# Performance work log

Hardware: AMD Instinct MI355X
Metric: run time of the kernel (lower is better)

Reference implementation:

```python
import jax, jax.numpy as jnp
import numpy as np
from jax import lax


def _lstm_last(x, Wih, Whh, bih, bhh):
    """Single-layer torch-style LSTM (gate order i,f,g,o); returns last hidden state.
    x: (M, T, F) -> (M, H)."""
    gx = jnp.einsum('mtf,gf->mtg', x, Wih) + bih + bhh  # precompute input contributions
    H = Whh.shape[1]
    Wh = Whh.T
    def step(carry, g):
        h, c = carry
        z = g + h @ Wh
        i, f, gg, o = jnp.split(z, 4, axis=-1)
        c = jax.nn.sigmoid(f) * c + jax.nn.sigmoid(i) * jnp.tanh(gg)
        h = jax.nn.sigmoid(o) * jnp.tanh(c)
        return (h, c), None
    M = x.shape[0]
    init = (jnp.zeros((M, H), x.dtype), jnp.zeros((M, H), x.dtype))
    (h, _), _ = lax.scan(step, init, jnp.swapaxes(gx, 0, 1))
    return h


def _forward(input_data, rel_encoding, lstm_Wih, lstm_Whh, lstm_bih, lstm_bhh,
             hop_w1, hop_b1, hop_w2, hop_b2, fn_w1, fn_b1, fn_w2, fn_b2):
    B, W, N, F = input_data.shape
    U = lstm_Whh.shape[1]
    # SequentialEmbedding: per-stock LSTM over the window, take last step
    x = jnp.transpose(input_data, (0, 2, 1, 3)).reshape(B * N, W, F)
    seq = _lstm_last(x, lstm_Wih, lstm_Whh, lstm_bih, lstm_bhh).reshape(B, N, U)

    # RelationalEmbedding: dense N x N k-hop message passing
    mask = (rel_encoding.sum(-1) > 0).astype(seq.dtype)  # (N,N)
    D = mask.sum(-1)                                      # (N,) degrees (self-loops keep >0)
    e = seq
    for k in range(hop_w1.shape[0]):  # k_hops: small fixed loop
        W1 = hop_w1[k]
        # mask * concat([e_i, e_j, enc]) @ W1 + b1, computed blockwise without
        # materializing the (B,N,N,2U+K) concat; mask scales only the pre-bias term
        xi = e @ W1[:U]                                    # (B,N,INP)
        xj = e @ W1[U:2 * U]                               # (B,N,INP)
        xe = jnp.einsum('ijk,kp->ijp', rel_encoding, W1[2 * U:])  # (N,N,INP)
        pre = mask[None, :, :, None] * (xi[:, :, None, :] + xj[:, None, :, :] + xe[None]) + hop_b1[k]
        hdn = jax.nn.leaky_relu(pre)                       # (B,N,N,INP)
        wts = jax.nn.leaky_relu(hdn @ hop_w2[k] + hop_b2[k])[..., 0]  # (B,N,N)
        scaled = (wts * mask) / D[None, :, None]
        # torch: sum_i scaled[b,i,j] * e_j  ==  e_j * (sum_i scaled[b,i,j])
        e = scaled.sum(axis=1)[..., None] * e

    # FullyConnected head: Linear(2U,2U)+LeakyReLU, Linear(2U,1)+LeakyReLU, squeeze
    comb = jnp.concatenate([seq, e], axis=-1)              # (B,N,2U)
    out = jax.nn.leaky_relu(comb @ fn_w1 + fn_b1)
    out = jax.nn.leaky_relu(out @ fn_w2 + fn_b2)
    return out[..., 0]                                     # (B,N)


def setup_inputs() -> dict:
    key = jax.random.key(0)
    ks = jax.random.split(key, 14)
    B, W, N, F = 2, 32, 768, 4
    U, K, KH = 32, 8, 2
    INP = 2 * U + K  # 72
    def w(k, shape, fan):
        return jax.random.normal(k, shape, jnp.float32) / np.float32(np.sqrt(fan))
    enc = (jax.random.uniform(ks[1], (N, N, K)) < 0.05).astype(jnp.float32)
    # self-loops in relation channel 0 so every node has degree >= 1
    enc = enc.at[:, :, 0].set(jnp.maximum(enc[:, :, 0], jnp.eye(N, dtype=jnp.float32)))
    return {
        'input_data': jax.random.normal(ks[0], (B, W, N, F), jnp.float32),
        'rel_encoding': enc,
        'lstm_Wih': w(ks[2], (4 * U, F), F),
        'lstm_Whh': w(ks[3], (4 * U, U), U),
        'lstm_bih': 0.01 * jax.random.normal(ks[4], (4 * U,), jnp.float32),
        'lstm_bhh': 0.01 * jax.random.normal(ks[5], (4 * U,), jnp.float32),
        'hop_w1': w(ks[6], (KH, INP, INP), INP),
        'hop_b1': 0.01 * jax.random.normal(ks[7], (KH, INP), jnp.float32),
        'hop_w2': w(ks[8], (KH, INP, 1), INP),
        'hop_b2': 0.01 * jax.random.normal(ks[9], (KH, 1), jnp.float32),
        'fn_w1': w(ks[10], (2 * U, 2 * U), 2 * U),
        'fn_b1': 0.01 * jax.random.normal(ks[11], (2 * U,), jnp.float32),
        'fn_w2': w(ks[12], (2 * U, 1), 2 * U),
        'fn_b2': 0.01 * jax.random.normal(ks[13], (1,), jnp.float32),
    }


def reference(input_data, rel_encoding, lstm_Wih, lstm_Whh, lstm_bih, lstm_bhh,
              hop_w1, hop_b1, hop_w2, hop_b2, fn_w1, fn_b1, fn_w2, fn_b2):
    return _forward(input_data, rel_encoding, lstm_Wih, lstm_Whh, lstm_bih, lstm_bhh,
                    hop_w1, hop_b1, hop_w2, hop_b2, fn_w1, fn_b1, fn_w2, fn_b2)
```

## Files before the change

kernel.cpp:

```cpp
#include <hip/hip_runtime.h>

#define N_STK 768
#define BATCH 2
#define WIN   32
#define FEAT  4
#define UNITS 32
#define INP   72
#define LROW  76
#define NSLC  19
#define IPH   64
#define JCR   24
#define NPHI  12
#define NCR   32

__device__ __forceinline__ float lrelu(float v){ return v > 0.0f ? v : 0.01f*v; }
__device__ __forceinline__ float lanebcast(float v, int l){
    return __int_as_float(__builtin_amdgcn_readlane(__float_as_int(v), l));
}
__device__ __forceinline__ unsigned patof(const float* __restrict__ p){
    float4 a = *reinterpret_cast<const float4*>(p);
    float4 b = *reinterpret_cast<const float4*>(p + 4);
    unsigned m = 0;
    m |= (a.x != 0.0f) ? 1u   : 0u;
    m |= (a.y != 0.0f) ? 2u   : 0u;
    m |= (a.z != 0.0f) ? 4u   : 0u;
    m |= (a.w != 0.0f) ? 8u   : 0u;
    m |= (b.x != 0.0f) ? 16u  : 0u;
    m |= (b.y != 0.0f) ? 32u  : 0u;
    m |= (b.z != 0.0f) ? 64u  : 0u;
    m |= (b.w != 0.0f) ? 128u : 0u;
    return m;
}
__device__ __forceinline__ void async_cp16(const float* g, float* l){
    __builtin_amdgcn_global_load_lds(
        (const __attribute__((address_space(1))) unsigned int*)g,
        (__attribute__((address_space(3))) unsigned int*)l,
        16, 0, 0);
}

__global__ __launch_bounds__(256) void k1_kernel(const float* __restrict__ rel,
        const float* __restrict__ x, const float* __restrict__ Wih,
        const float* __restrict__ Whh, const float* __restrict__ bih,
        const float* __restrict__ bhh, const float* __restrict__ hop_w1,
        const float* __restrict__ hop_b1,
        float* __restrict__ seq, float* __restrict__ invD,
        unsigned char* __restrict__ Pout,
        float* __restrict__ lutlo, float* __restrict__ luthi,
        float* __restrict__ xi0, float* __restrict__ xj0,
        float* __restrict__ s0){
    int j = blockIdx.x, tid = threadIdx.x;
    int wv = tid >> 6, lane = tid & 63;
    __shared__ float hrow[2][UNITS];
    __shared__ int cw_sh[2];

    if (wv < 2){
        int b = wv;
        int r0 = lane, r1 = 64 + lane;
        bool low = (lane < 32);
        float4 wi0 = *reinterpret_cast<const float4*>(Wih + r0*FEAT);
        float4 wi1 = *reinterpret_cast<const float4*>(Wih + r1*FEAT);
        float bb0 = bih[r0] + bhh[r0];
        float bb1 = bih[r1] + bhh[r1];
        float4 W0[8], W1[8];
        #pragma unroll
        for (int q = 0; q < 8; q++){
            W0[q] = *reinterpret_cast<const float4*>(Whh + r0*UNITS + q*4);
            W1[q] = *reinterpret_cast<const float4*>(Whh + r1*UNITS + q*4);
        }
        float4 xv = make_float4(0.f, 0.f, 0.f, 0.f);
        if (low) xv = *reinterpret_cast<const float4*>(x + ((size_t)(b*WIN + lane)*N_STK + j)*FEAT);
        float hreg = 0.0f, c = 0.0f;
        #pragma unroll 1
        for (int t = 0; t < WIN; t++){
            float xb0 = lanebcast(xv.x, t), xb1 = lanebcast(xv.y, t);
            float xb2 = lanebcast(xv.z, t), xb3 = lanebcast(xv.w, t);
            float z0a = bb0 + wi0.x*xb0 + wi0.z*xb2;
            float z0b =       wi0.y*xb1 + wi0.w*xb3;
            float z1a = bb1 + wi1.x*xb0 + wi1.z*xb2;
            float z1b =       wi1.y*xb1 + wi1.w*xb3;
            #pragma unroll
            for (int q = 0; q < 8; q++){
                float h0 = lanebcast(hreg, 32 + q*4 + 0);
                float h1 = lanebcast(hreg, 32 + q*4 + 1);
                float h2 = lanebcast(hreg, 32 + q*4 + 2);
                float h3 = lanebcast(hreg, 32 + q*4 + 3);
                z0a += W0[q].x*h0; z0b += W0[q].y*h1;
                z0a += W0[q].z*h2; z0b += W0[q].w*h3;
                z1a += W1[q].x*h0; z1b += W1[q].y*h1;
                z1a += W1[q].z*h2; z1b += W1[q].w*h3;
            }
            float z0 = z0a + z0b, z1 = z1a + z1b;
            float e0 = __expf(-z0);
            float s0g = 1.0f/(1.0f + e0);
            float sc = low ? -2.0f : -1.0f;
            float e1 = __expf(sc*z1);
            float rr = 1.0f/(1.0f + e1);
            float act = low ? (1.0f - e1)*rr : rr;
            float pa = s0g*act;
            float po = __shfl_xor(pa, 32);
            c = s0g*c + po;
            float e2 = __expf(-2.0f*c);
            float th = (1.0f - e2)/(1.0f + e2);
            hreg = act*th;
        }
        if (!low){
            hrow[b][lane - 32] = hreg;
            seq[((size_t)b*N_STK + j)*UNITS + (lane - 32)] = hreg;
        }
    } else {
        int half = wv - 2;
        int local = 0;
        #pragma unroll
        for (int k = 0; k < 6; k++){
            int col = half*384 + k*64 + lane;
            unsigned p = patof(rel + ((size_t)j*N_STK + col)*8);
            Pout[(size_t)j*N_STK + col] = (unsigned char)p;
            local += p ? 1 : 0;
        }
        #pragma unroll
        for (int d = 32; d; d >>= 1) local += __shfl_xor(local, d);
        if (lane == 0) cw_sh[half] = local;
    }
    __syncthreads();
    if (tid == 0){
        invD[j] = 1.0f/(float)(cw_sh[0] + cw_sh[1]);
        s0[j] = 0.0f; s0[N_STK + j] = 0.0f;
    }
    if (j < 64 && tid >= 144 && tid < 216){
        int p = tid - 144;
        int m = j & 15, half = (j >> 4) & 1, k = j >> 5;
        const float* W = hop_w1 + (size_t)k*INP*INP;
        float acc = half ? 0.0f : hop_b1[k*INP + p];
        int base = 2*UNITS + (half ? 4 : 0);
        #pragma unroll
        for (int q = 0; q < 4; q++)
            if ((m >> q) & 1) acc += W[(base + q)*INP + p];
        (half ? luthi : lutlo)[(k*16 + m)*INP + p] = acc;
    }
    if (tid < 2*INP){
        int b = tid/INP, p = tid - b*INP;
        float si = 0.0f, sj = 0.0f;
        #pragma unroll
        for (int u = 0; u < UNITS; u++){
            float ev = hrow[b][u];
            si += ev * hop_w1[u*INP + p];
            sj += ev * hop_w1[(UNITS + u)*INP + p];
        }
        size_t o = ((size_t)b*N_STK + j)*INP + p;
        xi0[o] = si; xj0[o] = sj;
    }
}

__global__ __launch_bounds__(256) void hop_kernel(const float* __restrict__ xi,
        const float* __restrict__ xj,
        const float* __restrict__ lutlo_k, const float* __restrict__ luthi_k,
        const float* __restrict__ w2, const float* __restrict__ b2,
        const unsigned char* __restrict__ P, const float* __restrict__ invD,
        float* __restrict__ s_out){
    int cr = blockIdx.x, ip = blockIdx.y, b = blockIdx.z;
    int j0 = cr*JCR, i0 = ip*IPH, tid = threadIdx.x;
    __shared__ float xi_sh[IPH*LROW];
    __shared__ float xj_sh[JCR*LROW];
    __shared__ float lo_sh[16*LROW];
    __shared__ float hi_sh[16*LROW];
    __shared__ float invD_sh[IPH];
    __shared__ float acc_sh[JCR];
    __shared__ unsigned elist[IPH*JCR];
    __shared__ int lcnt;

    const float* xib = xi + ((size_t)b*N_STK + i0)*INP;
    const float* xjb = xj + ((size_t)b*N_STK + j0)*INP;

    if (tid == 0) lcnt = 0;
    if (tid < JCR) acc_sh[tid] = 0.0f;
    __syncthreads();

    for (int u = tid; u < IPH*NSLC; u += 256){
        int r = u/NSLC, sl = u - r*NSLC;
        int off = (sl < 18) ? sl*4 : 0;
        async_cp16(xib + (size_t)r*INP + off, &xi_sh[0] + (size_t)u*4);
    }
    for (int u = tid; u < JCR*NSLC; u += 256){
        int r = u/NSLC, sl = u - r*NSLC;
        int off = (sl < 18) ? sl*4 : 0;
        async_cp16(xjb + (size_t)r*INP + off, &xj_sh[0] + (size_t)u*4);
    }
    for (int u = tid; u < 16*NSLC; u += 256){
        int r = u/NSLC, sl = u - r*NSLC;
        int off = (sl < 18) ? sl*4 : 0;
        async_cp16(lutlo_k + r*INP + off, &lo_sh[0] + (size_t)u*4);
    }
    for (int u = tid; u < 16*NSLC; u += 256){
        int r = u/NSLC, sl = u - r*NSLC;
        int off = (sl < 18) ? sl*4 : 0;
        async_cp16(luthi_k + r*INP + off, &hi_sh[0] + (size_t)u*4);
    }
    if (tid < IPH/4) async_cp16(invD + i0 + tid*4, &invD_sh[0] + tid*4);

    if (tid < IPH){
        const unsigned* prow = reinterpret_cast<const unsigned*>(P + (size_t)(i0 + tid)*N_STK + j0);
        unsigned w[6];
        #pragma unroll
        for (int k = 0; k < 6; k++) w[k] = prow[k];
        #pragma unroll
        for (int k = 0; k < 24; k++){
            unsigned pat = (w[k >> 2] >> ((k & 3)*8)) & 255u;
            if (pat){
                int pos = atomicAdd(&lcnt, 1);
                elist[pos] = ((unsigned)tid << 13) | ((unsigned)k << 8) | pat;
            }
        }
    }

    int hf = tid & 1;
    float4 w2r[9];
    #pragma unroll
    for (int q = 0; q < 9; q++) w2r[q] = *reinterpret_cast<const float4*>(w2 + hf*36 + q*4);
    float b2v = b2[0];
    __syncthreads();

    int m = lcnt;
    for (int sl = tid >> 1; sl < m; sl += 128){
        unsigned ent = elist[sl];
        int il = ent >> 13, jl = (ent >> 8) & 31;
        int mlo = (int)(ent & 15u), mhi = (int)((ent >> 4) & 15u);
        const float* xr = &xi_sh[il*LROW + hf*36];
        const float* jr = &xj_sh[jl*LROW + hf*36];
        const float* lr = &lo_sh[mlo*LROW + hf*36];
        const float* hr = &hi_sh[mhi*LROW + hf*36];
        float dot = 0.0f;
        #pragma unroll
        for (int q = 0; q < 9; q++){
            float4 xv = *reinterpret_cast<const float4*>(xr + q*4);
            float4 jv = *reinterpret_cast<const float4*>(jr + q*4);
            float4 lv = *reinterpret_cast<const float4*>(lr + q*4);
            float4 hv = *reinterpret_cast<const float4*>(hr + q*4);
            float4 w  = w2r[q];
            dot += lrelu(xv.x + jv.x + lv.x + hv.x)*w.x;
            dot += lrelu(xv.y + jv.y + lv.y + hv.y)*w.y;
            dot += lrelu(xv.z + jv.z + lv.z + hv.z)*w.z;
            dot += lrelu(xv.w + jv.w + lv.w + hv.w)*w.w;
        }
        dot += __shfl_xor(dot, 1);
        if (hf == 0) atomicAdd(&acc_sh[jl], lrelu(dot + b2v)*invD_sh[il]);
    }
    __syncthreads();
    if (tid < JCR) atomicAdd(&s_out[b*N_STK + j0 + tid], acc_sh[tid]);
}

template<int MODE>
__global__ __launch_bounds__(192) void ep_kernel(const float* __restrict__ sview,
        const float* __restrict__ ein, const float* __restrict__ seqg,
        float* __restrict__ eout,
        const float* __restrict__ W1next, float* __restrict__ xi_next,
        float* __restrict__ xj_next, float* __restrict__ s_next,
        const float* __restrict__ fw1, const float* __restrict__ fb1,
        const float* __restrict__ fw2, const float* __restrict__ fb2,
        float* __restrict__ outp){
    int j = blockIdx.x, tid = threadIdx.x;
    __shared__ float e_sh[2][64];
    if (tid < 64){
        int b = tid >> 5, u = tid & 31;
        size_t o = ((size_t)b*N_STK + j)*UNITS + u;
        float ev = ein[o]*sview[b*N_STK + j];
        if (MODE == 0){ e_sh[b][u] = ev; eout[o] = ev; }
        else          { e_sh[b][32 + u] = ev; e_sh[b][u] = seqg[o]; }
    }
    if (MODE == 0 && tid >= 160 && tid < 162) s_next[(tid - 160)*N_STK + j] = 0.0f;
    __syncthreads();
    if (MODE == 0){
        if (tid < 2*INP){
            int b = tid/INP, p = tid - b*INP;
            float si = 0.0f, sj = 0.0f;
            #pragma unroll
            for (int u = 0; u < UNITS; u++){
                float ev = e_sh[b][u];
                si += ev * W1next[u*INP + p];
                sj += ev * W1next[(UNITS + u)*INP + p];
            }
            size_t o = ((size_t)b*N_STK + j)*INP + p;
            xi_next[o] = si; xj_next[o] = sj;
        }
    } else {
        if (tid < 128){
            int b = tid >> 6, u = tid & 63;
            float acc = fb1[u];
            #pragma unroll 8
            for (int d = 0; d < 64; d++) acc += e_sh[b][d]*fw1[d*64 + u];
            float prod = lrelu(acc)*fw2[u];
            prod += __shfl_xor(prod, 32);
            prod += __shfl_xor(prod, 16);
            prod += __shfl_xor(prod, 8);
            prod += __shfl_xor(prod, 4);
            prod += __shfl_xor(prod, 2);
            prod += __shfl_xor(prod, 1);
            if (u == 0) outp[b*N_STK + j] = lrelu(prod + fb2[0]);
        }
    }
}

extern "C" void kernel_launch(void* const* d_in, const int* in_sizes, int n_in,
                              void* d_out, int out_size, void* d_ws, size_t ws_size,
                              hipStream_t stream){
    const float* input_data = (const float*)d_in[0];
    const float* rel        = (const float*)d_in[1];
    const float* lstm_Wih   = (const float*)d_in[2];
    const float* lstm_Whh   = (const float*)d_in[3];
    const float* lstm_bih   = (const float*)d_in[4];
    const float* lstm_bhh   = (const float*)d_in[5];
    const float* hop_w1     = (const float*)d_in[6];
    const float* hop_b1     = (const float*)d_in[7];
    const float* hop_w2     = (const float*)d_in[8];
    const float* hop_b2     = (const float*)d_in[9];
    const float* fn_w1      = (const float*)d_in[10];
    const float* fn_b1      = (const float*)d_in[11];
    const float* fn_w2      = (const float*)d_in[12];
    const float* fn_b2      = (const float*)d_in[13];
    float* out = (float*)d_out;

    float* ws    = (float*)d_ws;
    float* seq   = ws;
    float* eA    = seq   + 49152;
    float* xi0   = eA    + 49152;
    float* xj0   = xi0   + 110592;
    float* xi1   = xj0   + 110592;
    float* xj1   = xi1   + 110592;
    float* lutlo = xj1   + 110592;
    float* luthi = lutlo + 2304;
    float* invD  = luthi + 2304;
    float* s0    = invD  + 768;
    float* s1    = s0    + 1536;
    unsigned char* P = (unsigned char*)(s1 + 1536);

    k1_kernel<<<N_STK, 256, 0, stream>>>(rel, input_data, lstm_Wih, lstm_Whh,
            lstm_bih, lstm_bhh, hop_w1, hop_b1,
            seq, invD, P, lutlo, luthi, xi0, xj0, s0);

    dim3 hgrid(NCR, NPHI, BATCH);
    hop_kernel<<<hgrid, 256, 0, stream>>>(xi0, xj0, lutlo, luthi,
            hop_w2, hop_b2, P, invD, s0);

    ep_kernel<0><<<N_STK, 192, 0, stream>>>(s0, seq, nullptr, eA,
            hop_w1 + INP*INP, xi1, xj1, s1,
            nullptr, nullptr, nullptr, nullptr, nullptr);

    hop_kernel<<<hgrid, 256, 0, stream>>>(xi1, xj1, lutlo + 16*INP, luthi + 16*INP,
            hop_w2 + INP, hop_b2 + 1, P, invD, s1);

    ep_kernel<1><<<N_STK, 192, 0, stream>>>(s1, eA, seq, nullptr,
            nullptr, nullptr, nullptr, nullptr,
            fn_w1, fn_b1, fn_w2, fn_b2, out);
}
```

Measured before the change: 148.6 us.

## Fuse epilogue kernels into hop kernel via last-block counter and split edge lists

Removes the two separate epilogue kernel launches by having the last hop block for each column range (found with a global atomic counter after a threadfence) run the epilogue work for its 24 columns. The edge list is now built with a deterministic wave prefix scan, split into low-only patterns (one LUT row) and patterns that need both LUTs, so low-only edges skip the second LUT lookup. Counter and s1 zeroing move into k1. This trades launch overhead for serialized tail work in a few blocks and adds atomic and fence costs.

```diff
diff --git a/kernel.cpp b/kernel.cpp
--- a/kernel.cpp
+++ b/kernel.cpp
@@ -47,7 +47,8 @@
         unsigned char* __restrict__ Pout,
         float* __restrict__ lutlo, float* __restrict__ luthi,
         float* __restrict__ xi0, float* __restrict__ xj0,
-        float* __restrict__ s0){
+        float* __restrict__ s0, float* __restrict__ s1,
+        int* __restrict__ cnt0, int* __restrict__ cnt1){
     int j = blockIdx.x, tid = threadIdx.x;
     int wv = tid >> 6, lane = tid & 63;
     __shared__ float hrow[2][UNITS];
@@ -91,14 +92,14 @@
             }
             float z0 = z0a + z0b, z1 = z1a + z1b;
             float e0 = __expf(-z0);
-            float s0g = 1.0f/(1.0f + e0);
+            float sg = 1.0f/(1.0f + e0);
             float sc = low ? -2.0f : -1.0f;
             float e1 = __expf(sc*z1);
             float rr = 1.0f/(1.0f + e1);
             float act = low ? (1.0f - e1)*rr : rr;
-            float pa = s0g*act;
+            float pa = sg*act;
             float po = __shfl_xor(pa, 32);
-            c = s0g*c + po;
+            c = sg*c + po;
             float e2 = __expf(-2.0f*c);
             float th = (1.0f - e2)/(1.0f + e2);
             hreg = act*th;
@@ -113,9 +114,9 @@
         #pragma unroll
         for (int k = 0; k < 6; k++){
             int col = half*384 + k*64 + lane;
-            unsigned p = patof(rel + ((size_t)j*N_STK + col)*8);
-            Pout[(size_t)j*N_STK + col] = (unsigned char)p;
-            local += p ? 1 : 0;
+            unsigned pt = patof(rel + ((size_t)j*N_STK + col)*8);
+            Pout[(size_t)j*N_STK + col] = (unsigned char)pt;
+            local += pt ? 1 : 0;
         }
         #pragma unroll
         for (int d = 32; d; d >>= 1) local += __shfl_xor(local, d);
@@ -125,38 +126,47 @@
     if (tid == 0){
         invD[j] = 1.0f/(float)(cw_sh[0] + cw_sh[1]);
         s0[j] = 0.0f; s0[N_STK + j] = 0.0f;
-    }
+        s1[j] = 0.0f; s1[N_STK + j] = 0.0f;
+    }
+    if (j < 64 && tid == 1){ cnt0[j] = 0; cnt1[j] = 0; }
     if (j < 64 && tid >= 144 && tid < 216){
-        int p = tid - 144;
+        int pp = tid - 144;
         int m = j & 15, half = (j >> 4) & 1, k = j >> 5;
         const float* W = hop_w1 + (size_t)k*INP*INP;
-        float acc = half ? 0.0f : hop_b1[k*INP + p];
+        float acc = half ? 0.0f : hop_b1[k*INP + pp];
         int base = 2*UNITS + (half ? 4 : 0);
         #pragma unroll
         for (int q = 0; q < 4; q++)
-            if ((m >> q) & 1) acc += W[(base + q)*INP + p];
-        (half ? luthi : lutlo)[(k*16 + m)*INP + p] = acc;
+            if ((m >> q) & 1) acc += W[(base + q)*INP + pp];
+        (half ? luthi : lutlo)[(k*16 + m)*INP + pp] = acc;
     }
     if (tid < 2*INP){
-        int b = tid/INP, p = tid - b*INP;
+        int b = tid/INP, pp = tid - b*INP;
         float si = 0.0f, sj = 0.0f;
         #pragma unroll
         for (int u = 0; u < UNITS; u++){
             float ev = hrow[b][u];
-            si += ev * hop_w1[u*INP + p];
-            sj += ev * hop_w1[(UNITS + u)*INP + p];
-        }
-        size_t o = ((size_t)b*N_STK + j)*INP + p;
+            si += ev * hop_w1[u*INP + pp];
+            sj += ev * hop_w1[(UNITS + u)*INP + pp];
+        }
+        size_t o = ((size_t)b*N_STK + j)*INP + pp;
         xi0[o] = si; xj0[o] = sj;
     }
 }
 
+template<int MODE>
 __global__ __launch_bounds__(256) void hop_kernel(const float* __restrict__ xi,
         const float* __restrict__ xj,
         const float* __restrict__ lutlo_k, const float* __restrict__ luthi_k,
         const float* __restrict__ w2, const float* __restrict__ b2,
         const unsigned char* __restrict__ P, const float* __restrict__ invD,
-        float* __restrict__ s_out){
+        float* __restrict__ s_out, int* __restrict__ cnt,
+        const float* __restrict__ seqg, float* __restrict__ eA,
+        const float* __restrict__ W1next, float* __restrict__ xi_next,
+        float* __restrict__ xj_next,
+        const float* __restrict__ fw1, const float* __restrict__ fb1,
+        const float* __restrict__ fw2, const float* __restrict__ fb2,
+        float* __restrict__ outp){
     int cr = blockIdx.x, ip = blockIdx.y, b = blockIdx.z;
     int j0 = cr*JCR, i0 = ip*IPH, tid = threadIdx.x;
     __shared__ float xi_sh[IPH*LROW];
@@ -165,15 +175,13 @@
     __shared__ float hi_sh[16*LROW];
     __shared__ float invD_sh[IPH];
     __shared__ float acc_sh[JCR];
+    __shared__ float sarr[JCR];
     __shared__ unsigned elist[IPH*JCR];
-    __shared__ int lcnt;
+    __shared__ int n0_sh, nt_sh, isLast;
 
     const float* xib = xi + ((size_t)b*N_STK + i0)*INP;
     const float* xjb = xj + ((size_t)b*N_STK + j0)*INP;
-
-    if (tid == 0) lcnt = 0;
-    if (tid < JCR) acc_sh[tid] = 0.0f;
-    __syncthreads();
+    if (tid >= 224 && tid < 224 + JCR) acc_sh[tid - 224] = 0.0f;
 
     for (int u = tid; u < IPH*NSLC; u += 256){
         int r = u/NSLC, sl = u - r*NSLC;
@@ -197,19 +205,35 @@
     }
     if (tid < IPH/4) async_cp16(invD + i0 + tid*4, &invD_sh[0] + tid*4);
 
-    if (tid < IPH){
+    if (tid < 64){
         const unsigned* prow = reinterpret_cast<const unsigned*>(P + (size_t)(i0 + tid)*N_STK + j0);
         unsigned w[6];
         #pragma unroll
         for (int k = 0; k < 6; k++) w[k] = prow[k];
+        int c0 = 0, c1 = 0;
         #pragma unroll
         for (int k = 0; k < 24; k++){
             unsigned pat = (w[k >> 2] >> ((k & 3)*8)) & 255u;
-            if (pat){
-                int pos = atomicAdd(&lcnt, 1);
-                elist[pos] = ((unsigned)tid << 13) | ((unsigned)k << 8) | pat;
-            }
-        }
+            c0 += (pat && pat < 16u) ? 1 : 0;
+            c1 += (pat >= 16u) ? 1 : 0;
+        }
+        int s0v = c0, s1v = c1;
+        #pragma unroll
+        for (int off = 1; off < 64; off <<= 1){
+            int a0 = __shfl_up(s0v, off), a1 = __shfl_up(s1v, off);
+            if (tid >= off){ s0v += a0; s1v += a1; }
+        }
+        int N0 = __shfl(s0v, 63);
+        int Nt = N0 + __shfl(s1v, 63);
+        int p0 = s0v - c0, p1 = N0 + s1v - c1;
+        #pragma unroll
+        for (int k = 0; k < 24; k++){
+            unsigned pat = (w[k >> 2] >> ((k & 3)*8)) & 255u;
+            unsigned enc = ((unsigned)tid << 13) | ((unsigned)k << 8) | pat;
+            if (pat && pat < 16u) elist[p0++] = enc;
+            else if (pat >= 16u)  elist[p1++] = enc;
+        }
+        if (tid == 0){ n0_sh = N0; nt_sh = Nt; }
     }
 
     int hf = tid & 1;
@@ -219,8 +243,29 @@
     float b2v = b2[0];
     __syncthreads();
 
-    int m = lcnt;
-    for (int sl = tid >> 1; sl < m; sl += 128){
+    int n0 = n0_sh, ntot = nt_sh;
+    for (int sl = tid >> 1; sl < n0; sl += 128){
+        unsigned ent = elist[sl];
+        int il = ent >> 13, jl = (ent >> 8) & 31, mlo = (int)(ent & 15u);
+        const float* xr = &xi_sh[il*LROW + hf*36];
+        const float* jr = &xj_sh[jl*LROW + hf*36];
+        const float* lr = &lo_sh[mlo*LROW + hf*36];
+        float dot = 0.0f;
+        #pragma unroll
+        for (int q = 0; q < 9; q++){
+            float4 xv = *reinterpret_cast<const float4*>(xr + q*4);
+            float4 jv = *reinterpret_cast<const float4*>(jr + q*4);
+            float4 lv = *reinterpret_cast<const float4*>(lr + q*4);
+            float4 w  = w2r[q];
+            dot += lrelu(xv.x + jv.x + lv.x)*w.x;
+            dot += lrelu(xv.y + jv.y + lv.y)*w.y;
+            dot += lrelu(xv.z + jv.z + lv.z)*w.z;
+            dot += lrelu(xv.w + jv.w + lv.w)*w.w;
+        }
+        dot += __shfl_xor(dot, 1);
+        if (hf == 0) atomicAdd(&acc_sh[jl], lrelu(dot + b2v)*invD_sh[il]);
+    }
+    for (int sl = n0 + (tid >> 1); sl < ntot; sl += 128){
         unsigned ent = elist[sl];
         int il = ent >> 13, jl = (ent >> 8) & 31;
         int mlo = (int)(ent & 15u), mhi = (int)((ent >> 4) & 15u);
@@ -246,55 +291,63 @@
     }
     __syncthreads();
     if (tid < JCR) atomicAdd(&s_out[b*N_STK + j0 + tid], acc_sh[tid]);
-}
-
-template<int MODE>
-__global__ __launch_bounds__(192) void ep_kernel(const float* __restrict__ sview,
-        const float* __restrict__ ein, const float* __restrict__ seqg,
-        float* __restrict__ eout,
-        const float* __restrict__ W1next, float* __restrict__ xi_next,
-        float* __restrict__ xj_next, float* __restrict__ s_next,
-        const float* __restrict__ fw1, const float* __restrict__ fb1,
-        const float* __restrict__ fw2, const float* __restrict__ fb2,
-        float* __restrict__ outp){
-    int j = blockIdx.x, tid = threadIdx.x;
-    __shared__ float e_sh[2][64];
-    if (tid < 64){
-        int b = tid >> 5, u = tid & 31;
-        size_t o = ((size_t)b*N_STK + j)*UNITS + u;
-        float ev = ein[o]*sview[b*N_STK + j];
-        if (MODE == 0){ e_sh[b][u] = ev; eout[o] = ev; }
-        else          { e_sh[b][32 + u] = ev; e_sh[b][u] = seqg[o]; }
-    }
-    if (MODE == 0 && tid >= 160 && tid < 162) s_next[(tid - 160)*N_STK + j] = 0.0f;
-    __syncthreads();
+
+    __threadfence();
+    __syncthreads();
+    if (tid == 0){
+        int old = atomicAdd(&cnt[b*NCR + cr], 1);
+        isLast = (old == NPHI - 1) ? 1 : 0;
+    }
+    __syncthreads();
+    if (!isLast) return;
+
+    if (tid < JCR) sarr[tid] = atomicAdd(&s_out[b*N_STK + j0 + tid], 0.0f);
+    __syncthreads();
+
     if (MODE == 0){
-        if (tid < 2*INP){
-            int b = tid/INP, p = tid - b*INP;
+        float* es = xi_sh;
+        for (int idx = tid; idx < JCR*UNITS; idx += 256){
+            int c = idx >> 5, u = idx & 31;
+            size_t o = ((size_t)b*N_STK + j0 + c)*UNITS + u;
+            float ev = seqg[o]*sarr[c];
+            eA[o] = ev;
+            es[idx] = ev;
+        }
+        __syncthreads();
+        for (int idx = tid; idx < JCR*INP; idx += 256){
+            int c = idx/INP, pp = idx - c*INP;
             float si = 0.0f, sj = 0.0f;
             #pragma unroll
             for (int u = 0; u < UNITS; u++){
-                float ev = e_sh[b][u];
-                si += ev * W1next[u*INP + p];
-                sj += ev * W1next[(UNITS + u)*INP + p];
+                float ev = es[c*UNITS + u];
+                si += ev * W1next[u*INP + pp];
+                sj += ev * W1next[(UNITS + u)*INP + pp];
             }
-            size_t o = ((size_t)b*N_STK + j)*INP + p;
+            size_t o = ((size_t)b*N_STK + j0 + c)*INP + pp;
             xi_next[o] = si; xj_next[o] = sj;
         }
     } else {
-        if (tid < 128){
-            int b = tid >> 6, u = tid & 63;
+        float* comb = xi_sh;
+        float* parr = xi_sh + JCR*64;
+        for (int idx = tid; idx < JCR*64; idx += 256){
+            int c = idx >> 6, d = idx & 63;
+            size_t o = ((size_t)b*N_STK + j0 + c)*UNITS;
+            comb[idx] = (d < 32) ? seqg[o + d] : eA[o + d - 32]*sarr[c];
+        }
+        __syncthreads();
+        for (int idx = tid; idx < JCR*64; idx += 256){
+            int c = idx >> 6, u = idx & 63;
             float acc = fb1[u];
             #pragma unroll 8
-            for (int d = 0; d < 64; d++) acc += e_sh[b][d]*fw1[d*64 + u];
-            float prod = lrelu(acc)*fw2[u];
-            prod += __shfl_xor(prod, 32);
-            prod += __shfl_xor(prod, 16);
-            prod += __shfl_xor(prod, 8);
-            prod += __shfl_xor(prod, 4);
-            prod += __shfl_xor(prod, 2);
-            prod += __shfl_xor(prod, 1);
-            if (u == 0) outp[b*N_STK + j] = lrelu(prod + fb2[0]);
+            for (int d = 0; d < 64; d++) acc += comb[c*64 + d]*fw1[d*64 + u];
+            parr[idx] = lrelu(acc)*fw2[u];
+        }
+        __syncthreads();
+        if (tid < JCR){
+            float s = 0.0f;
+            #pragma unroll 8
+            for (int u = 0; u < 64; u++) s += parr[tid*64 + u];
+            outp[b*N_STK + j0 + tid] = lrelu(s + fb2[0]);
         }
     }
 }
@@ -330,24 +383,22 @@
     float* invD  = luthi + 2304;
     float* s0    = invD  + 768;
     float* s1    = s0    + 1536;
-    unsigned char* P = (unsigned char*)(s1 + 1536);
+    int*   cnt0  = (int*)(s1 + 1536);
+    int*   cnt1  = cnt0  + 64;
+    unsigned char* P = (unsigned char*)(cnt1 + 64);
 
     k1_kernel<<<N_STK, 256, 0, stream>>>(rel, input_data, lstm_Wih, lstm_Whh,
             lstm_bih, lstm_bhh, hop_w1, hop_b1,
-            seq, invD, P, lutlo, luthi, xi0, xj0, s0);
+            seq, invD, P, lutlo, luthi, xi0, xj0, s0, s1, cnt0, cnt1);
 
     dim3 hgrid(NCR, NPHI, BATCH);
-    hop_kernel<<<hgrid, 256, 0, stream>>>(xi0, xj0, lutlo, luthi,
-            hop_w2, hop_b2, P, invD, s0);
-
-    ep_kernel<0><<<N_STK, 192, 0, stream>>>(s0, seq, nullptr, eA,
-            hop_w1 + INP*INP, xi1, xj1, s1,
+    hop_kernel<0><<<hgrid, 256, 0, stream>>>(xi0, xj0, lutlo, luthi,
+            hop_w2, hop_b2, P, invD, s0, cnt0,
+            seq, eA, hop_w1 + INP*INP, xi1, xj1,
             nullptr, nullptr, nullptr, nullptr, nullptr);
 
-    hop_kernel<<<hgrid, 256, 0, stream>>>(xi1, xj1, lutlo + 16*INP, luthi + 16*INP,
-            hop_w2 + INP, hop_b2 + 1, P, invD, s1);
-
-    ep_kernel<1><<<N_STK, 192, 0, stream>>>(s1, eA, seq, nullptr,
-            nullptr, nullptr, nullptr, nullptr,
+    hop_kernel<1><<<hgrid, 256, 0, stream>>>(xi1, xj1, lutlo + 16*INP, luthi + 16*INP,
+            hop_w2 + INP, hop_b2 + 1, P, invD, s1, cnt1,
+            seq, eA, nullptr, nullptr, nullptr,
             fn_w1, fn_b1, fn_w2, fn_b2, out);
 }
```

Result: slower. 239.5 us (+61.2%).

## Partition edge list by high-nibble pattern and skip the high LUT when zero

Applied to the files above, without the earlier changes.

The hop kernel now builds its edge list with a wave-level prefix scan instead of shared-memory atomics. Edges whose relation pattern has no bits in the upper nibble go first, so a specialised loop can skip the high-LUT load and add for them. The i-tile also shrinks from 64 to 48 rows with more blocks along i, which cuts shared memory per block and raises block count. The costs are two loop bodies instead of one and more duplicated loads of the j-side and LUT data across the extra blocks.

```diff
diff --git a/kernel.cpp b/kernel.cpp
--- a/kernel.cpp
+++ b/kernel.cpp
@@ -8,9 +8,9 @@
 #define INP   72
 #define LROW  76
 #define NSLC  19
-#define IPH   64
+#define IPH   48
 #define JCR   24
-#define NPHI  12
+#define NPHI  16
 #define NCR   32
 
 __device__ __forceinline__ float lrelu(float v){ return v > 0.0f ? v : 0.01f*v; }
@@ -91,14 +91,14 @@
             }
             float z0 = z0a + z0b, z1 = z1a + z1b;
             float e0 = __expf(-z0);
-            float s0g = 1.0f/(1.0f + e0);
+            float sg = 1.0f/(1.0f + e0);
             float sc = low ? -2.0f : -1.0f;
             float e1 = __expf(sc*z1);
             float rr = 1.0f/(1.0f + e1);
             float act = low ? (1.0f - e1)*rr : rr;
-            float pa = s0g*act;
+            float pa = sg*act;
             float po = __shfl_xor(pa, 32);
-            c = s0g*c + po;
+            c = sg*c + po;
             float e2 = __expf(-2.0f*c);
             float th = (1.0f - e2)/(1.0f + e2);
             hreg = act*th;
@@ -113,9 +113,9 @@
         #pragma unroll
         for (int k = 0; k < 6; k++){
             int col = half*384 + k*64 + lane;
-            unsigned p = patof(rel + ((size_t)j*N_STK + col)*8);
-            Pout[(size_t)j*N_STK + col] = (unsigned char)p;
-            local += p ? 1 : 0;
+            unsigned pt = patof(rel + ((size_t)j*N_STK + col)*8);
+            Pout[(size_t)j*N_STK + col] = (unsigned char)pt;
+            local += pt ? 1 : 0;
         }
         #pragma unroll
         for (int d = 32; d; d >>= 1) local += __shfl_xor(local, d);
@@ -127,26 +127,26 @@
         s0[j] = 0.0f; s0[N_STK + j] = 0.0f;
     }
     if (j < 64 && tid >= 144 && tid < 216){
-        int p = tid - 144;
+        int pp = tid - 144;
         int m = j & 15, half = (j >> 4) & 1, k = j >> 5;
         const float* W = hop_w1 + (size_t)k*INP*INP;
-        float acc = half ? 0.0f : hop_b1[k*INP + p];
+        float acc = half ? 0.0f : hop_b1[k*INP + pp];
         int base = 2*UNITS + (half ? 4 : 0);
         #pragma unroll
         for (int q = 0; q < 4; q++)
-            if ((m >> q) & 1) acc += W[(base + q)*INP + p];
-        (half ? luthi : lutlo)[(k*16 + m)*INP + p] = acc;
+            if ((m >> q) & 1) acc += W[(base + q)*INP + pp];
+        (half ? luthi : lutlo)[(k*16 + m)*INP + pp] = acc;
     }
     if (tid < 2*INP){
-        int b = tid/INP, p = tid - b*INP;
+        int b = tid/INP, pp = tid - b*INP;
         float si = 0.0f, sj = 0.0f;
         #pragma unroll
         for (int u = 0; u < UNITS; u++){
             float ev = hrow[b][u];
-            si += ev * hop_w1[u*INP + p];
-            sj += ev * hop_w1[(UNITS + u)*INP + p];
-        }
-        size_t o = ((size_t)b*N_STK + j)*INP + p;
+            si += ev * hop_w1[u*INP + pp];
+            sj += ev * hop_w1[(UNITS + u)*INP + pp];
+        }
+        size_t o = ((size_t)b*N_STK + j)*INP + pp;
         xi0[o] = si; xj0[o] = sj;
     }
 }
@@ -166,14 +166,11 @@
     __shared__ float invD_sh[IPH];
     __shared__ float acc_sh[JCR];
     __shared__ unsigned elist[IPH*JCR];
-    __shared__ int lcnt;
+    __shared__ int n0_sh, nt_sh;
 
     const float* xib = xi + ((size_t)b*N_STK + i0)*INP;
     const float* xjb = xj + ((size_t)b*N_STK + j0)*INP;
-
-    if (tid == 0) lcnt = 0;
-    if (tid < JCR) acc_sh[tid] = 0.0f;
-    __syncthreads();
+    if (tid >= 224 && tid < 224 + JCR) acc_sh[tid - 224] = 0.0f;
 
     for (int u = tid; u < IPH*NSLC; u += 256){
         int r = u/NSLC, sl = u - r*NSLC;
@@ -197,19 +194,39 @@
     }
     if (tid < IPH/4) async_cp16(invD + i0 + tid*4, &invD_sh[0] + tid*4);
 
-    if (tid < IPH){
-        const unsigned* prow = reinterpret_cast<const unsigned*>(P + (size_t)(i0 + tid)*N_STK + j0);
-        unsigned w[6];
-        #pragma unroll
-        for (int k = 0; k < 6; k++) w[k] = prow[k];
-        #pragma unroll
-        for (int k = 0; k < 24; k++){
-            unsigned pat = (w[k >> 2] >> ((k & 3)*8)) & 255u;
-            if (pat){
-                int pos = atomicAdd(&lcnt, 1);
-                elist[pos] = ((unsigned)tid << 13) | ((unsigned)k << 8) | pat;
+    if (tid < 64){
+        unsigned w[6] = {0,0,0,0,0,0};
+        int c0 = 0, c1 = 0;
+        if (tid < IPH){
+            const unsigned* prow = reinterpret_cast<const unsigned*>(P + (size_t)(i0 + tid)*N_STK + j0);
+            #pragma unroll
+            for (int k = 0; k < 6; k++) w[k] = prow[k];
+            #pragma unroll
+            for (int k = 0; k < 24; k++){
+                unsigned pat = (w[k >> 2] >> ((k & 3)*8)) & 255u;
+                c0 += (pat && pat < 16u) ? 1 : 0;
+                c1 += (pat >= 16u) ? 1 : 0;
             }
         }
+        int s0v = c0, s1v = c1;
+        #pragma unroll
+        for (int off = 1; off < 64; off <<= 1){
+            int a0 = __shfl_up(s0v, off), a1 = __shfl_up(s1v, off);
+            if (tid >= off){ s0v += a0; s1v += a1; }
+        }
+        int N0 = __shfl(s0v, 63);
+        int Nt = N0 + __shfl(s1v, 63);
+        if (tid < IPH){
+            int p0 = s0v - c0, p1 = N0 + s1v - c1;
+            #pragma unroll
+            for (int k = 0; k < 24; k++){
+                unsigned pat = (w[k >> 2] >> ((k & 3)*8)) & 255u;
+                unsigned enc = ((unsigned)tid << 13) | ((unsigned)k << 8) | pat;
+                if (pat && pat < 16u) elist[p0++] = enc;
+                else if (pat >= 16u)  elist[p1++] = enc;
+            }
+        }
+        if (tid == 0){ n0_sh = N0; nt_sh = Nt; }
     }
 
     int hf = tid & 1;
@@ -219,8 +236,29 @@
     float b2v = b2[0];
     __syncthreads();
 
-    int m = lcnt;
-    for (int sl = tid >> 1; sl < m; sl += 128){
+    int n0 = n0_sh, ntot = nt_sh;
+    for (int sl = tid >> 1; sl < n0; sl += 128){
+        unsigned ent = elist[sl];
+        int il = ent >> 13, jl = (ent >> 8) & 31, mlo = (int)(ent & 15u);
+        const float* xr = &xi_sh[il*LROW + hf*36];
+        const float* jr = &xj_sh[jl*LROW + hf*36];
+        const float* lr = &lo_sh[mlo*LROW + hf*36];
+        float dot = 0.0f;
+        #pragma unroll
+        for (int q = 0; q < 9; q++){
+            float4 xv = *reinterpret_cast<const float4*>(xr + q*4);
+            float4 jv = *reinterpret_cast<const float4*>(jr + q*4);
+            float4 lv = *reinterpret_cast<const float4*>(lr + q*4);
+            float4 w  = w2r[q];
+            dot += lrelu(xv.x + jv.x + lv.x)*w.x;
+            dot += lrelu(xv.y + jv.y + lv.y)*w.y;
+            dot += lrelu(xv.z + jv.z + lv.z)*w.z;
+            dot += lrelu(xv.w + jv.w + lv.w)*w.w;
+        }
+        dot += __shfl_xor(dot, 1);
+        if (hf == 0) atomicAdd(&acc_sh[jl], lrelu(dot + b2v)*invD_sh[il]);
+    }
+    for (int sl = n0 + (tid >> 1); sl < ntot; sl += 128){
         unsigned ent = elist[sl];
         int il = ent >> 13, jl = (ent >> 8) & 31;
         int mlo = (int)(ent & 15u), mhi = (int)((ent >> 4) & 15u);
@@ -270,15 +308,15 @@
     __syncthreads();
     if (MODE == 0){
         if (tid < 2*INP){
-            int b = tid/INP, p = tid - b*INP;
+            int b = tid/INP, pp = tid - b*INP;
             float si = 0.0f, sj = 0.0f;
             #pragma unroll
             for (int u = 0; u < UNITS; u++){
                 float ev = e_sh[b][u];
-                si += ev * W1next[u*INP + p];
-                sj += ev * W1next[(UNITS + u)*INP + p];
+                si += ev * W1next[u*INP + pp];
+                sj += ev * W1next[(UNITS + u)*INP + pp];
             }
-            size_t o = ((size_t)b*N_STK + j)*INP + p;
+            size_t o = ((size_t)b*N_STK + j)*INP + pp;
             xi_next[o] = si; xj_next[o] = sj;
         }
     } else {
```

Result: no change. 147.5 us (-0.8%).
